# Performance work log

Hardware: AMD Instinct MI355X
Metric: run time of the kernel (lower is better)

## Reference

```python
import jax, jax.numpy as jnp
import numpy as np

N = 100000      # n_nodes
E = 1600000     # n_edges (avg degree 16)
IN_C = 256
OUT_C = 64
HID = OUT_C * 2  # 128


def setup_inputs() -> dict:
    key = jax.random.key(0)
    k = jax.random.split(key, 4)
    x = jax.random.normal(k[0], (N, IN_C), dtype=jnp.float32)
    edge_index = jax.random.randint(k[1], (2, E), 0, N, dtype=jnp.int64)
    W1 = jax.random.normal(k[2], (IN_C, HID), dtype=jnp.float32) * (1.0 / np.sqrt(IN_C))
    b1 = jnp.zeros((HID,), dtype=jnp.float32)
    W2 = jax.random.normal(k[3], (HID, OUT_C), dtype=jnp.float32) * (1.0 / np.sqrt(HID))
    b2 = jnp.zeros((OUT_C,), dtype=jnp.float32)
    return {"x": x, "edge_index": edge_index, "W1": W1, "b1": b1, "W2": W2, "b2": b2}


def reference(x, edge_index, W1, b1, W2, b2):
    n = x.shape[0]
    # GCNConv default: add self-loops, symmetric normalization D^-1/2 A D^-1/2
    loop = jnp.arange(n, dtype=edge_index.dtype)
    src = jnp.concatenate([edge_index[0], loop])  # [E+N]
    dst = jnp.concatenate([edge_index[1], loop])  # [E+N]
    deg = jax.ops.segment_sum(jnp.ones_like(dst, dtype=x.dtype), dst, num_segments=n)
    dis = jax.lax.rsqrt(deg)  # deg >= 1 thanks to self-loops
    norm = dis[src] * dis[dst]  # [E+N]

    def gcn_conv(h, W, b):
        h = h @ W                                   # [n, d_out] dense transform first
        msg = h[src] * norm[:, None]                # [E+N, d_out] gather + scale
        return jax.ops.segment_sum(msg, dst, num_segments=n) + b

    h = jax.nn.relu(gcn_conv(x, W1, b1))
    return gcn_conv(h, W2, b2)
```

## Files before the change

kernel.cpp:

```cpp
#include <hip/hip_runtime.h>
#include <hip/hip_bf16.h>


#define GCN_IN_C 256
#define GCN_HID  128
#define GCN_OUT  64

#define BKT_SHIFT 8
#define BKT_NODES 256
#define EPB 4096

typedef __bf16 bf16x8 __attribute__((ext_vector_type(8)));
typedef float f32x4 __attribute__((ext_vector_type(4)));

__global__ __launch_bounds__(256) void k_zero_i32(int* __restrict__ p, int n) {
  int i = blockIdx.x * 256 + threadIdx.x;
  if (i < n) p[i] = 0;
}

__global__ __launch_bounds__(256) void k_bucket_hist(const int* __restrict__ dst,
                                                     int* __restrict__ bcnt, int e, int nb) {
  __shared__ int h[512];
  int tid = threadIdx.x;
  h[tid] = 0; h[tid + 256] = 0;
  __syncthreads();
  int base = blockIdx.x * EPB;
#pragma unroll
  for (int j = 0; j < EPB / 256; ++j) {
    int i = base + j * 256 + tid;
    if (i < e) atomicAdd(&h[dst[i] >> BKT_SHIFT], 1);
  }
  __syncthreads();
  if (tid < nb && h[tid]) atomicAdd(&bcnt[tid], h[tid]);
  if (tid + 256 < nb && h[tid + 256]) atomicAdd(&bcnt[tid + 256], h[tid + 256]);
}

__global__ __launch_bounds__(512) void k_scan_buckets(const int* __restrict__ bcnt,
                                                      int* __restrict__ bbase,
                                                      int* __restrict__ bcur, int nb) {
  __shared__ int sh[512];
  int t = threadIdx.x;
  int v = (t < nb) ? bcnt[t] : 0;
  sh[t] = v;
  __syncthreads();
  for (int d = 1; d < 512; d <<= 1) {
    int x = (t >= d) ? sh[t - d] : 0;
    __syncthreads();
    sh[t] += x;
    __syncthreads();
  }
  if (t < nb) {
    int ex = sh[t] - v;
    bbase[t] = ex;
    bcur[t] = ex;
  }
}

__global__ __launch_bounds__(256) void k_partition(const int* __restrict__ src,
                                                   const int* __restrict__ dst,
                                                   int* __restrict__ bcur,
                                                   unsigned int* __restrict__ part,
                                                   int e, int nb) {
  __shared__ int h[512];
  __shared__ int base[512];
  int tid = threadIdx.x;
  h[tid] = 0; h[tid + 256] = 0;
  __syncthreads();
  int b0 = blockIdx.x * EPB;
  int s[EPB / 256], d[EPB / 256], rk[EPB / 256];
#pragma unroll
  for (int j = 0; j < EPB / 256; ++j) {
    int i = b0 + j * 256 + tid;
    if (i < e) {
      s[j] = src[i];
      d[j] = dst[i];
      rk[j] = atomicAdd(&h[d[j] >> BKT_SHIFT], 1);
    }
  }
  __syncthreads();
  if (tid < nb && h[tid]) base[tid] = atomicAdd(&bcur[tid], h[tid]);
  if (tid + 256 < nb && h[tid + 256]) base[tid + 256] = atomicAdd(&bcur[tid + 256], h[tid + 256]);
  __syncthreads();
#pragma unroll
  for (int j = 0; j < EPB / 256; ++j) {
    int i = b0 + j * 256 + tid;
    if (i < e) {
      int bk = d[j] >> BKT_SHIFT;
      unsigned int dl = (unsigned int)(d[j] & (BKT_NODES - 1));
      part[base[bk] + rk[j]] = (dl << 24) | (unsigned int)s[j];
    }
  }
}

__global__ __launch_bounds__(256) void k_bucket_csr(
    const unsigned int* __restrict__ part, const int* __restrict__ bbase,
    const int* __restrict__ bcnt, int* __restrict__ off, int* __restrict__ end,
    float* __restrict__ dis, int* __restrict__ csr, int n) {
  __shared__ int cnt[256];
  __shared__ int sc[256];
  __shared__ int cur[256];
  int b = blockIdx.x, tid = threadIdx.x;
  int node0 = b << BKT_SHIFT;
  int eb0 = bbase[b];
  int ebn = bcnt[b];
  cnt[tid] = 0;
  __syncthreads();
  for (int i = tid; i < ebn; i += 256) atomicAdd(&cnt[part[eb0 + i] >> 24], 1);
  __syncthreads();
  int v = cnt[tid];
  sc[tid] = v;
  __syncthreads();
  for (int dd = 1; dd < 256; dd <<= 1) {
    int x = (tid >= dd) ? sc[tid - dd] : 0;
    __syncthreads();
    sc[tid] += x;
    __syncthreads();
  }
  int lo = sc[tid] - v;
  cur[tid] = lo;
  int node = node0 + tid;
  if (node < n) {
    off[node] = eb0 + lo;
    end[node] = eb0 + lo + v;
    dis[node] = rsqrtf((float)v + 1.0f);
  }
  __syncthreads();
  for (int i = tid; i < ebn; i += 256) {
    unsigned int u = part[eb0 + i];
    int r = atomicAdd(&cur[u >> 24], 1);
    csr[eb0 + r] = (int)(u & 0xFFFFFFu);
  }
}

template<int K, int NOUT>
__global__ __launch_bounds__(256) void k_split_w(const float* __restrict__ W,
                                                 __bf16* __restrict__ Wsp) {
  constexpr int KSTEPS = K / 32;
  int idx = blockIdx.x * 256 + threadIdx.x;
  if (idx >= KSTEPS * 4 * NOUT) return;
  int n = idx % NOUT;
  int g = (idx / NOUT) & 3;
  int ks = idx / (4 * NOUT);
  __bf16* hi = Wsp + (size_t)ks * (2 * 4 * NOUT * 8) + ((size_t)g * NOUT + n) * 8;
  __bf16* lo = hi + 4 * NOUT * 8;
#pragma unroll
  for (int j = 0; j < 8; ++j) {
    float f = W[(size_t)(ks * 32 + g * 8 + j) * NOUT + n];
    __bf16 h = (__bf16)f;
    hi[j] = h;
    lo[j] = (__bf16)(f - (float)h);
  }
}

template<int K, int NOUT, bool IN_RELU_BIAS>
__global__ __launch_bounds__(256) void k_gemm_mfma(
    const float* __restrict__ X, const __bf16* __restrict__ Wsp,
    const float* __restrict__ inb, const float* __restrict__ dis,
    __bf16* __restrict__ T, int M) {
  constexpr int BM = 128;
  constexpr int NF = NOUT / 16;
  constexpr int KSTEPS = K / 32;
  constexpr int TILE = 2 * 4 * NOUT * 8;
  constexpr int GRAN = TILE * 2 / 16;
  constexpr int GPT = GRAN / 256;
  __shared__ __bf16 blds[2][TILE];

  const int tid = threadIdx.x;
  const int wave = tid >> 6;
  const int lane = tid & 63;
  const int l15 = lane & 15;
  const int lg = lane >> 4;
  const int r0w = blockIdx.x * BM + wave * 32;

  f32x4 acc[2][NF];
#pragma unroll
  for (int mf = 0; mf < 2; ++mf)
#pragma unroll
    for (int nf = 0; nf < NF; ++nf) acc[mf][nf] = (f32x4){0.f, 0.f, 0.f, 0.f};

  int rowA[2];
#pragma unroll
  for (int mf = 0; mf < 2; ++mf) {
    int r = r0w + mf * 16 + l15;
    rowA[mf] = (r < M) ? r : (M - 1);
  }

  const uint4* gW = (const uint4*)Wsp;
  {
    uint4* dst4 = (uint4*)&blds[0][0];
#pragma unroll
    for (int i = 0; i < GPT; ++i) dst4[tid + i * 256] = gW[tid + i * 256];
  }
  __syncthreads();

  int cur = 0;
  for (int ks = 0; ks < KSTEPS; ++ks) {
    uint4 sreg[GPT];
    if (ks + 1 < KSTEPS) {
#pragma unroll
      for (int i = 0; i < GPT; ++i)
        sreg[i] = gW[(size_t)(ks + 1) * GPT * 256 + tid + i * 256];
    }
    bf16x8 ah[2], al[2];
    const int k0 = ks * 32 + lg * 8;
#pragma unroll
    for (int mf = 0; mf < 2; ++mf) {
      const float* ap = X + (size_t)rowA[mf] * K + k0;
      float4 v0 = *(const float4*)ap;
      float4 v1 = *(const float4*)(ap + 4);
      float va[8] = {v0.x, v0.y, v0.z, v0.w, v1.x, v1.y, v1.z, v1.w};
      if (IN_RELU_BIAS) {
        float4 bb0 = *(const float4*)(inb + k0);
        float4 bb1 = *(const float4*)(inb + k0 + 4);
        float bb[8] = {bb0.x, bb0.y, bb0.z, bb0.w, bb1.x, bb1.y, bb1.z, bb1.w};
#pragma unroll
        for (int j = 0; j < 8; ++j) va[j] = fmaxf(va[j] + bb[j], 0.f);
      }
#pragma unroll
      for (int j = 0; j < 8; ++j) {
        __bf16 h = (__bf16)va[j];
        ah[mf][j] = h;
        al[mf][j] = (__bf16)(va[j] - (float)h);
      }
    }
    const __bf16* bh_base = &blds[cur][0];
    const __bf16* bl_base = &blds[cur][4 * NOUT * 8];
    const int boff = lg * NOUT * 8 + l15 * 8;
#pragma unroll
    for (int nf = 0; nf < NF; ++nf) {
      bf16x8 bh = *(const bf16x8*)(bh_base + boff + nf * 128);
      bf16x8 bl = *(const bf16x8*)(bl_base + boff + nf * 128);
#pragma unroll
      for (int mf = 0; mf < 2; ++mf) {
        acc[mf][nf] = __builtin_amdgcn_mfma_f32_16x16x32_bf16(ah[mf], bh, acc[mf][nf], 0, 0, 0);
        acc[mf][nf] = __builtin_amdgcn_mfma_f32_16x16x32_bf16(ah[mf], bl, acc[mf][nf], 0, 0, 0);
        acc[mf][nf] = __builtin_amdgcn_mfma_f32_16x16x32_bf16(al[mf], bh, acc[mf][nf], 0, 0, 0);
      }
    }
    if (ks + 1 < KSTEPS) {
      uint4* dst4 = (uint4*)&blds[cur ^ 1][0];
#pragma unroll
      for (int i = 0; i < GPT; ++i) dst4[tid + i * 256] = sreg[i];
    }
    __syncthreads();
    cur ^= 1;
  }

#pragma unroll
  for (int mf = 0; mf < 2; ++mf) {
    int rbase = r0w + mf * 16 + lg * 4;
    float dv[4];
#pragma unroll
    for (int r = 0; r < 4; ++r) dv[r] = (rbase + r < M) ? dis[rbase + r] : 0.f;
#pragma unroll
    for (int nf = 0; nf < NF; ++nf) {
#pragma unroll
      for (int r = 0; r < 4; ++r) {
        int rr = rbase + r;
        if (rr < M) T[(size_t)rr * NOUT + nf * 16 + l15] = (__bf16)(dv[r] * acc[mf][nf][r]);
      }
    }
  }
}

template<int C, bool BIAS>
__global__ __launch_bounds__(256) void k_agg_csr(
    const int* __restrict__ csr, const int* __restrict__ off,
    const int* __restrict__ end, const __bf16* __restrict__ ts,
    const float* __restrict__ dis, const float* __restrict__ bias,
    float* __restrict__ out, int n) {
  constexpr int LPG = C / 8;
  constexpr int G = 64 / LPG;
  int wid = (blockIdx.x * 256 + threadIdx.x) >> 6;
  int lane = threadIdx.x & 63;
  int gid = lane / LPG;
  int gl = lane % LPG;
  if (wid >= n) return;

  float acc[8];
#pragma unroll
  for (int j = 0; j < 8; ++j) acc[j] = 0.f;
  if (gid == 0) {
    bf16x8 v = *(const bf16x8*)(ts + (size_t)wid * C + gl * 8);
#pragma unroll
    for (int j = 0; j < 8; ++j) acc[j] = (float)v[j];
  }

  int e = off[wid] + gid;
  int e1 = end[wid];
  for (; e + G < e1; e += 2 * G) {
    int s0 = csr[e];
    int s1 = csr[e + G];
    bf16x8 v0 = *(const bf16x8*)(ts + (size_t)s0 * C + gl * 8);
    bf16x8 v1 = *(const bf16x8*)(ts + (size_t)s1 * C + gl * 8);
#pragma unroll
    for (int j = 0; j < 8; ++j) acc[j] += (float)v0[j] + (float)v1[j];
  }
  if (e < e1) {
    int s0 = csr[e];
    bf16x8 v0 = *(const bf16x8*)(ts + (size_t)s0 * C + gl * 8);
#pragma unroll
    for (int j = 0; j < 8; ++j) acc[j] += (float)v0[j];
  }

#pragma unroll
  for (int w = LPG; w < 64; w <<= 1) {
#pragma unroll
    for (int j = 0; j < 8; ++j) acc[j] += __shfl_xor(acc[j], w);
  }

  if (gid == 0) {
    float di = dis[wid];
    float o[8];
#pragma unroll
    for (int j = 0; j < 8; ++j) {
      o[j] = di * acc[j];
      if (BIAS) o[j] += bias[gl * 8 + j];
    }
    float4* op = (float4*)(out + (size_t)wid * C + gl * 8);
    op[0] = make_float4(o[0], o[1], o[2], o[3]);
    op[1] = make_float4(o[4], o[5], o[6], o[7]);
  }
}

extern "C" void kernel_launch(void* const* d_in, const int* in_sizes, int n_in,
                              void* d_out, int out_size, void* d_ws, size_t ws_size,
                              hipStream_t stream) {
  const float* x  = (const float*)d_in[0];
  const int*   ei = (const int*)d_in[1];
  const float* W1 = (const float*)d_in[2];
  const float* b1 = (const float*)d_in[3];
  const float* W2 = (const float*)d_in[4];
  const float* b2 = (const float*)d_in[5];
  float* out = (float*)d_out;

  const int N = in_sizes[0] / GCN_IN_C;
  const int E = in_sizes[1] / 2;
  const int* src = ei;
  const int* dst = ei + E;
  const int NB = (N + BKT_NODES - 1) >> BKT_SHIFT;
  const int EB = (E + EPB - 1) / EPB;

  char* p = (char*)d_ws;
  float* dis = (float*)p;             p += (size_t)N * 4;
  __bf16* t1s = (__bf16*)p;           p += (size_t)N * GCN_HID * 2;
  float* a1  = (float*)p;             p += (size_t)N * GCN_HID * 4;
  int* off   = (int*)p;               p += (size_t)N * 4;
  int* end   = (int*)p;               p += (size_t)N * 4;
  int* csr   = (int*)p;               p += (size_t)E * 4;
  int* bcnt  = (int*)p;               p += 512 * 4;
  int* bbase = (int*)p;               p += 512 * 4;
  int* bcur  = (int*)p;               p += 512 * 4;
  __bf16* w1sp = (__bf16*)p;          p += (size_t)(GCN_IN_C / 32) * 2 * 4 * GCN_HID * 8 * 2;
  __bf16* w2sp = (__bf16*)p;
  unsigned int* part = (unsigned int*)a1;
  __bf16* t2s = t1s;

  k_split_w<GCN_IN_C, GCN_HID>
      <<<((GCN_IN_C / 32) * 4 * GCN_HID + 255) / 256, 256, 0, stream>>>(W1, w1sp);
  k_split_w<GCN_HID, GCN_OUT>
      <<<((GCN_HID / 32) * 4 * GCN_OUT + 255) / 256, 256, 0, stream>>>(W2, w2sp);

  k_zero_i32<<<2, 256, 0, stream>>>(bcnt, 512);
  k_bucket_hist<<<EB, 256, 0, stream>>>(dst, bcnt, E, NB);
  k_scan_buckets<<<1, 512, 0, stream>>>(bcnt, bbase, bcur, NB);
  k_partition<<<EB, 256, 0, stream>>>(src, dst, bcur, part, E, NB);
  k_bucket_csr<<<NB, 256, 0, stream>>>(part, bbase, bcnt, off, end, dis, csr, N);

  k_gemm_mfma<GCN_IN_C, GCN_HID, false>
      <<<(N + 127) / 128, 256, 0, stream>>>(x, w1sp, nullptr, dis, t1s, N);
  k_agg_csr<GCN_HID, false>
      <<<((size_t)N * 64 + 255) / 256, 256, 0, stream>>>(csr, off, end, t1s, dis, nullptr, a1, N);

  k_gemm_mfma<GCN_HID, GCN_OUT, true>
      <<<(N + 127) / 128, 256, 0, stream>>>(a1, w2sp, b1, dis, t2s, N);
  k_agg_csr<GCN_OUT, true>
      <<<((size_t)N * 64 + 255) / 256, 256, 0, stream>>>(csr, off, end, t2s, dis, b2, out, N);
}
```

Baseline: 232.1 us.

## Stage weight tiles via global_load_lds and prefetch A tiles one step ahead

Weight tiles now go straight from global memory into LDS with the direct-to-LDS load builtin, so the old path through registers followed by explicit LDS stores is gone. The X (A operand) fragments for the next k-step are also loaded into registers one iteration early, software-pipelining the global loads against the MFMA work. The aim is to hide global-load latency in the GEMM kernels and cut register and LDS-store traffic. The cost is more live registers for the prefetched A values. Correctness depends on the per-wave LDS offsets of global_load_lds matching the tile layout and on the existing barrier being enough to order the async LDS writes.

```diff
diff --git a/kernel.cpp b/kernel.cpp
--- a/kernel.cpp
+++ b/kernel.cpp
@@ -161,8 +161,7 @@
   constexpr int NF = NOUT / 16;
   constexpr int KSTEPS = K / 32;
   constexpr int TILE = 2 * 4 * NOUT * 8;
-  constexpr int GRAN = TILE * 2 / 16;
-  constexpr int GPT = GRAN / 256;
+  constexpr int GPT = (TILE * 2) / 16 / 256;
   __shared__ __bf16 blds[2][TILE];
 
   const int tid = threadIdx.x;
@@ -185,30 +184,43 @@
     rowA[mf] = (r < M) ? r : (M - 1);
   }
 
-  const uint4* gW = (const uint4*)Wsp;
-  {
-    uint4* dst4 = (uint4*)&blds[0][0];
-#pragma unroll
-    for (int i = 0; i < GPT; ++i) dst4[tid + i * 256] = gW[tid + i * 256];
-  }
+  auto stage = [&](int ks, int b) {
+    const char* gs = (const char*)Wsp + (size_t)ks * TILE * 2 + (size_t)tid * 16;
+    char* ls = (char*)&blds[b][0] + wave * 1024;
+#pragma unroll
+    for (int i = 0; i < GPT; ++i) {
+      __builtin_amdgcn_global_load_lds(
+          (const __attribute__((address_space(1))) void*)(gs + i * 4096),
+          (__attribute__((address_space(3))) void*)(ls + i * 4096),
+          16, 0, 0);
+    }
+  };
+  auto loadA = [&](int ks, float4* v0, float4* v1) {
+#pragma unroll
+    for (int mf = 0; mf < 2; ++mf) {
+      const float* ap = X + (size_t)rowA[mf] * K + ks * 32 + lg * 8;
+      v0[mf] = *(const float4*)ap;
+      v1[mf] = *(const float4*)(ap + 4);
+    }
+  };
+
+  float4 ca0[2], ca1[2], na0[2], na1[2];
+  stage(0, 0);
+  loadA(0, ca0, ca1);
   __syncthreads();
 
   int cur = 0;
   for (int ks = 0; ks < KSTEPS; ++ks) {
-    uint4 sreg[GPT];
     if (ks + 1 < KSTEPS) {
-#pragma unroll
-      for (int i = 0; i < GPT; ++i)
-        sreg[i] = gW[(size_t)(ks + 1) * GPT * 256 + tid + i * 256];
+      stage(ks + 1, cur ^ 1);
+      loadA(ks + 1, na0, na1);
     }
     bf16x8 ah[2], al[2];
     const int k0 = ks * 32 + lg * 8;
 #pragma unroll
     for (int mf = 0; mf < 2; ++mf) {
-      const float* ap = X + (size_t)rowA[mf] * K + k0;
-      float4 v0 = *(const float4*)ap;
-      float4 v1 = *(const float4*)(ap + 4);
-      float va[8] = {v0.x, v0.y, v0.z, v0.w, v1.x, v1.y, v1.z, v1.w};
+      float va[8] = {ca0[mf].x, ca0[mf].y, ca0[mf].z, ca0[mf].w,
+                     ca1[mf].x, ca1[mf].y, ca1[mf].z, ca1[mf].w};
       if (IN_RELU_BIAS) {
         float4 bb0 = *(const float4*)(inb + k0);
         float4 bb1 = *(const float4*)(inb + k0 + 4);
@@ -237,13 +249,13 @@
         acc[mf][nf] = __builtin_amdgcn_mfma_f32_16x16x32_bf16(al[mf], bh, acc[mf][nf], 0, 0, 0);
       }
     }
-    if (ks + 1 < KSTEPS) {
-      uint4* dst4 = (uint4*)&blds[cur ^ 1][0];
-#pragma unroll
-      for (int i = 0; i < GPT; ++i) dst4[tid + i * 256] = sreg[i];
-    }
     __syncthreads();
     cur ^= 1;
+#pragma unroll
+    for (int mf = 0; mf < 2; ++mf) {
+      ca0[mf] = na0[mf];
+      ca1[mf] = na1[mf];
+    }
   }
 
 #pragma unroll
```

Result: slower. 242.2 us (+4.3%).
